# Kernel optimization log

Measured on AMD Instinct MI355X. Metric: run time of the kernel, lower is better.

## Reference

```python
import jax, jax.numpy as jnp
import numpy as np
import math

NUM_ITER = 5
FEAT_STRIDE = 16
GAUSS_SIGMA = 1.0
HINGE_THRESHOLD = -999.0
MIN_FILTER_REG = 1e-3
ALPHA_EPS = 0.0


def apply_filter(feat, weights):
    # feat: (ni, ns, C, H, W); weights: (ns, C, fH, fW) -> scores (ni, ns, oH, oW)
    ni, ns, C, H, W = feat.shape
    fH, fW = weights.shape[-2], weights.shape[-1]
    x = feat.reshape(ni, ns * C, H, W)
    out = jax.lax.conv_general_dilated(
        x, weights, window_strides=(1, 1),
        padding=((fH // 2, fH // 2), (fW // 2, fW // 2)),
        dimension_numbers=('NCHW', 'OIHW', 'NCHW'),
        feature_group_count=ns)
    return out  # (ni, ns, oH, oW); oH = H + (fH+1)%2


def get_label(center, out_sz, sigma):
    # center: (ni, ns, 2) in (row, col) order
    k0 = jnp.arange(out_sz[0], dtype=jnp.float32)[None, None, :, None]
    k1 = jnp.arange(out_sz[1], dtype=jnp.float32)[None, None, None, :]
    g0 = jnp.exp(-0.5 / (sigma * sigma) * (k0 - center[..., 0][..., None, None]) ** 2)
    g1 = jnp.exp(-0.5 / (sigma * sigma) * (k1 - center[..., 1][..., None, None]) ** 2)
    return g0 * g1  # (ni, ns, oH, oW)


def _forward(weights, feat, bb, log_step_length, filter_reg):
    ni, ns = feat.shape[0], feat.shape[1]
    fH, fW = weights.shape[-2], weights.shape[-1]
    out_sz = (feat.shape[-2] + (fH + 1) % 2, feat.shape[-1] + (fW + 1) % 2)
    step = jnp.exp(log_step_length)[0]
    reg = jnp.maximum(filter_reg * filter_reg, MIN_FILTER_REG ** 2)[0]
    dmap_offset = jnp.array([fH % 2, fW % 2], jnp.float32) / 2.0
    # (x, y) -> (row, col), feature-grid coordinates
    center = ((bb[..., :2] + bb[..., 2:] / 2.0) / FEAT_STRIDE)[..., ::-1] - dmap_offset
    label = get_label(center, out_sz, GAUSS_SIGMA)
    mask = (label > HINGE_THRESHOLD).astype(feat.dtype)
    label = label * mask
    sw = math.sqrt(1.0 / ni)

    losses = []
    for _ in range(NUM_ITER):
        scores = apply_filter(feat, weights)
        scores_act = mask * scores + (1.0 - mask) * jax.nn.relu(scores)
        score_mask = mask + (1.0 - mask) * (jax.lax.stop_gradient(scores) > 0).astype(scores.dtype)
        residuals = sw * (scores_act - label)
        losses.append((jnp.sum(residuals ** 2) + reg * jnp.sum(weights ** 2)) / ns)
        residuals_mapped = score_mask * (sw * residuals)
        # feat-transpose = adjoint of apply_filter w.r.t. the filter weights
        _, vjp_fn = jax.vjp(lambda w: apply_filter(feat, w), weights)
        data_grad = vjp_fn(residuals_mapped)[0]
        weights_grad = data_grad + reg * weights
        scores_grad = apply_filter(feat, weights_grad)
        scores_grad = sw * (score_mask * scores_grad)
        alpha_num = jnp.sum(weights_grad ** 2, axis=(1, 2, 3))  # (ns,)
        alpha_den = jnp.maximum(
            jnp.sum(scores_grad.reshape(ni, ns, -1) ** 2, axis=(0, 2))
            + (reg + ALPHA_EPS) * alpha_num, 1e-8)
        alpha = alpha_num / alpha_den
        weights = weights - step * alpha[:, None, None, None] * weights_grad

    scores = apply_filter(feat, weights)
    scores = mask * scores + (1.0 - mask) * jax.nn.relu(scores)
    losses.append((jnp.sum((sw * (scores - label)) ** 2) + reg * jnp.sum(weights ** 2)) / ns)
    return weights, jnp.stack(losses)


def setup_inputs() -> dict:
    key = jax.random.key(0)
    k1, k2, k3, k4 = jax.random.split(key, 4)
    ni, ns, C, H, W, fH, fW = 3, 32, 512, 22, 22, 4, 4
    weights = 0.01 * jax.random.normal(k1, (ns, C, fH, fW), jnp.float32)
    feat = jax.random.normal(k2, (ni, ns, C, H, W), jnp.float32)
    # boxes (x, y, w, h) in image coords (image size = 22*16 = 352)
    xy = jax.random.uniform(k3, (ni, ns, 2), jnp.float32, 50.0, 250.0)
    wh = jax.random.uniform(k4, (ni, ns, 2), jnp.float32, 32.0, 96.0)
    bb = jnp.concatenate([xy, wh], axis=-1)
    log_step_length = jnp.zeros((1,), jnp.float32)  # log(1.0)
    filter_reg = 0.01 * jnp.ones((1,), jnp.float32)
    return {"weights": weights, "feat": feat, "bb": bb,
            "log_step_length": log_step_length, "filter_reg": filter_reg}


def reference(weights, feat, bb, log_step_length, filter_reg):
    return _forward(weights, feat, bb, log_step_length, filter_reg)
```

## Files before the change

kernel.cpp:

```cpp
#include <hip/hip_runtime.h>
#include <hip/hip_fp16.h>

#define NI 3
#define NS 32
#define CHN 512
#define OH 23
#define P2 529
#define NP 50784
#define UV 484
#define WSZ 262144
#define KTOT 1536
#define RSP 1544

typedef unsigned int uint32;
typedef unsigned short u16;
typedef _Float16 h2 __attribute__((ext_vector_type(2)));
typedef _Float16 f16x8 __attribute__((ext_vector_type(8)));
typedef float f32x4 __attribute__((ext_vector_type(4)));

#define OFF_FEATT 0UL
#define OFF_LABEL 47579136UL
#define OFF_S0    47782272UL
#define OFF_S1    47985408UL
#define OFF_SGRAW 48188544UL
#define OFF_WG    48391680UL
#define OFF_WGF16 49440256UL
#define OFF_W0F16 49964544UL
#define OFF_PART  50488832UL
#define OFF_FEATC 50521600UL

#define P_DEN   0
#define P_NUM   4320
#define P_LOSS  5600
#define P_WSQ0  5760
#define P_WSQA  5792
#define P_WSQ5  6816
#define P_L5    7840

__device__ __forceinline__ float waveSum(float v) {
#pragma unroll
  for (int o = 32; o > 0; o >>= 1) v += __shfl_xor(v, o, 64);
  return v;
}

__device__ __forceinline__ float alphaFor(const float* __restrict__ part, int t, int s,
                                          float reg) {
  const float* np_ = part + P_NUM + (size_t)(t * NS + s) * 8;
  const float* dp_ = part + P_DEN + (size_t)(t * NS + s) * 6;
  float nu = 0.f;
#pragma unroll
  for (int i = 0; i < 8; ++i) nu += np_[i];
  float de = 0.f;
#pragma unroll
  for (int i = 0; i < 6; ++i) de += dp_[i];
  return nu / fmaxf(de + reg * nu, 1e-8f);
}

__global__ __launch_bounds__(256) void k_setup(const float* __restrict__ feat,
                                               const float* __restrict__ w0,
                                               const float* __restrict__ bb,
                                               u16* __restrict__ featT,
                                               u16* __restrict__ featC,
                                               u16* __restrict__ w0f16,
                                               float* __restrict__ wmaster,
                                               float* __restrict__ label,
                                               float* __restrict__ part) {
  __shared__ uint32 lds32[64 * 121];
  __shared__ float sred[4];
  int b = blockIdx.x, tid = threadIdx.x;
  if (b < 1536) {
    int snT = b >> 4, r4 = b & 15;
    int cb = r4 >> 1, uvh = r4 & 1;
    int s = snT / 3, n = snT % 3;
    const float* fsrc =
        feat + ((size_t)n * NS + s) * CHN * UV + (size_t)(cb * 64) * UV + uvh * 242;
#pragma unroll
    for (int it = 0; it < 31; ++it) {
      int idx = it * 256 + tid;
      if (idx < 7744) {
        int r = (unsigned)idx / 121u;
        int j = idx - r * 121;
        float2 v = *(const float2*)(fsrc + (size_t)r * UV + 2 * j);
        lds32[idx] = (uint32)__half_as_ushort(__float2half(v.x)) |
                     ((uint32)__half_as_ushort(__float2half(v.y)) << 16);
      }
    }
    __syncthreads();
    uint32* dstT = (uint32*)featT +
                   ((size_t)(snT * 4 + (cb >> 1)) * UV + uvh * 242) * 64 + (cb & 1) * 32;
#pragma unroll
    for (int it = 0; it < 16; ++it) {
      int o = it * 256 + tid;
      if (o < 3872) {
        int uv = o >> 4, kp = o & 15;
        int j = uv >> 1, sh = (uv & 1) * 16;
        uint32 a0 = lds32[(4 * kp + 0) * 121 + j];
        uint32 a1 = lds32[(4 * kp + 1) * 121 + j];
        uint32 a2 = lds32[(4 * kp + 2) * 121 + j];
        uint32 a3 = lds32[(4 * kp + 3) * 121 + j];
        uint2 val;
        val.x = ((a0 >> sh) & 0xffffu) | (((a1 >> sh) & 0xffffu) << 16);
        val.y = ((a2 >> sh) & 0xffffu) | (((a3 >> sh) & 0xffffu) << 16);
        *(uint2*)(dstT + (size_t)uv * 64 + 2 * kp) = val;
      }
    }
    uint32* dstC =
        (uint32*)featC + ((size_t)(s * CHN + cb * 64)) * 768 + n * 256 + uvh * 121;
    if (uvh == 0) {
#pragma unroll
      for (int it = 0; it < 31; ++it) {
        int idx = it * 256 + tid;
        if (idx < 7744) {
          int c = (unsigned)idx / 121u;
          int j = idx - c * 121;
          dstC[(size_t)c * 768 + j] = lds32[idx];
        }
      }
    } else {
#pragma unroll
      for (int it = 0; it < 34; ++it) {
        int idx = it * 256 + tid;
        if (idx < 8640) {
          int c = (unsigned)idx / 135u;
          int j = idx - c * 135;
          dstC[(size_t)c * 768 + j] = (j < 121) ? lds32[c * 121 + j] : 0u;
        }
      }
    }
  } else if (b < 1568) {
    int s = b - 1536;
    for (int i = tid; i < 8192; i += 256) {
      int tap = i >> 9, c = i & 511;
      w0f16[(size_t)s * 8192 + i] =
          __half_as_ushort(__float2half(w0[(size_t)s * 8192 + c * 16 + tap]));
    }
    float sq = 0.f;
    for (int i = tid; i < 8192; i += 256) {
      float v = w0[(size_t)s * 8192 + i];
      wmaster[(size_t)s * 8192 + i] = v;
      sq += v * v;
    }
    sq = waveSum(sq);
    if ((tid & 63) == 0) sred[tid >> 6] = sq;
    __syncthreads();
    if (tid == 0) part[P_WSQ0 + s] = sred[0] + sred[1] + sred[2] + sred[3];
  } else {
    int p = (b - 1568) * 256 + tid;
    if (p < NP) {
      int nsid = p / P2, rem = p % P2;
      int i = rem / OH, j = rem % OH;
      const float* bp = bb + (size_t)nsid * 4;
      float cr = (bp[1] + 0.5f * bp[3]) * 0.0625f;
      float cc = (bp[0] + 0.5f * bp[2]) * 0.0625f;
      float dy = (float)i - cr, dx = (float)j - cc;
      label[p] = __expf(-0.5f * (dy * dy + dx * dx));
    }
  }
}

__global__ __launch_bounds__(1024) void k_conv_fwd(const u16* __restrict__ featT,
                                                   const u16* __restrict__ wf16,
                                                   float* __restrict__ outbuf, int t,
                                                   float* __restrict__ part) {
  __shared__ uint32 w_lds[16 * 260];
  __shared__ float G[288 * 17];
  __shared__ float dred[16];
  int tid = threadIdx.x;
  int bidx = blockIdx.x;
  int snT = bidx >> 1, h = bidx & 1;
  int s = snT / 3, n = snT - s * 3;
  const uint32* wsrc = (const uint32*)(wf16 + (size_t)s * 8192);
  for (int i = tid; i < 4096; i += 1024) {
    int tap = i >> 8, p = i & 255;
    w_lds[tap * 260 + p] = wsrc[i];
  }
  __syncthreads();
  int wave = tid >> 6, lane = tid & 63;
  int q = lane >> 4, m16 = lane & 15;
  int uv0 = h ? 220 : 0;
  int ntiles = 18 - h;
  int t0 = wave;
  bool has2 = (wave + 16 < ntiles);
  int t1 = has2 ? wave + 16 : wave;
  f32x4 acc0 = {0.f, 0.f, 0.f, 0.f}, acc1 = {0.f, 0.f, 0.f, 0.f};
  size_t base = (size_t)snT * 4 * UV * 128;
  int r0i = uv0 + t0 * 16 + m16;
  if (r0i > 483) r0i = 483;
  int r1i = uv0 + t1 * 16 + m16;
  if (r1i > 483) r1i = 483;
  size_t row0 = (size_t)r0i * 128;
  size_t row1 = (size_t)r1i * 128;
#pragma unroll
  for (int step = 0; step < 16; ++step) {
    int cb = step >> 2, cin = (step & 3) * 32;
    size_t cbase = base + (size_t)cb * UV * 128 + cin + q * 8;
    f16x8 a0 = *(const f16x8*)(featT + cbase + row0);
    uint4 bw = *(const uint4*)&w_lds[m16 * 260 + step * 16 + q * 4];
    f16x8 bf = __builtin_bit_cast(f16x8, bw);
    acc0 = __builtin_amdgcn_mfma_f32_16x16x32_f16(a0, bf, acc0, 0, 0, 0);
    if (has2) {
      f16x8 a1 = *(const f16x8*)(featT + cbase + row1);
      acc1 = __builtin_amdgcn_mfma_f32_16x16x32_f16(a1, bf, acc1, 0, 0, 0);
    }
  }
#pragma unroll
  for (int r = 0; r < 4; ++r) G[(t0 * 16 + q * 4 + r) * 17 + m16] = acc0[r];
  if (has2) {
#pragma unroll
    for (int r = 0; r < 4; ++r) G[(t1 * 16 + q * 4 + r) * 17 + m16] = acc1[r];
  }
  __syncthreads();
  float dsq = 0.f;
  int y0 = h ? 12 : 0;
  int npix = h ? 253 : 276;
  int p = tid;
  if (p < npix) {
    int yl = p / 23, x = p - yl * 23;
    int y = y0 + yl;
    float val = 0.f;
#pragma unroll
    for (int ky = 0; ky < 4; ++ky) {
      int u = y + ky - 2;
      if ((unsigned)u < 22u) {
#pragma unroll
        for (int kx = 0; kx < 4; ++kx) {
          int v = x + kx - 2;
          if ((unsigned)v < 22u) val += G[(u * 22 + v - uv0) * 17 + ky * 4 + kx];
        }
      }
    }
    outbuf[(size_t)(n * NS + s) * P2 + y * 23 + x] = val;
    dsq = val * val;
  }
  if (t >= 0) {
    dsq = waveSum(dsq);
    if (lane == 0) dred[wave] = dsq;
    __syncthreads();
    if (tid == 0) {
      float dsum = 0.f;
#pragma unroll
      for (int i = 0; i < 16; ++i) dsum += dred[i];
      part[P_DEN + ((size_t)(t * NS + s) * 3 + n) * 2 + h] = dsum * (1.0f / 3.0f);
    }
  }
}

__global__ __launch_bounds__(1024) void k_adjoint(
    int t, const u16* __restrict__ featC, const float* __restrict__ label,
    const float* __restrict__ scores_old, float* __restrict__ scores_new,
    const float* __restrict__ sgraw, float* __restrict__ wg, u16* __restrict__ wgf16,
    float* __restrict__ wmaster, float* __restrict__ part, const float* __restrict__ lsl,
    const float* __restrict__ fr) {
  __shared__ float r_lds[3 * P2];
  __shared__ __align__(16) u16 rs[16 * RSP];
  __shared__ __align__(16) float kred[3 * 4 * 64 * 4];
  __shared__ float lred[16], nred[16], wred[16];
  int tid = threadIdx.x;
  int s = blockIdx.x >> 3, chunk = blockIdx.x & 7;
  int c0 = chunk * 64;
  float step = __expf(lsl[0]);
  float frv = fr[0];
  float reg = fmaxf(frv * frv, 1e-6f);
  float alpha_p = (t >= 1) ? alphaFor(part, t - 1, s, reg) : 0.f;

  float lsum = 0.f;
  for (int pl = tid; pl < 1587; pl += 1024) {
    int nn = (unsigned)pl / (unsigned)P2;
    int rem = pl - nn * P2;
    size_t gp = (size_t)(nn * NS + s) * P2 + rem;
    float S = scores_old[gp];
    if (t >= 1) S -= step * alpha_p * sgraw[gp];
    float d = S - label[gp];
    r_lds[nn * P2 + rem] = d * (1.0f / 3.0f);
    if (chunk == 0) {
      if (t >= 1) scores_new[gp] = S;
      lsum += d * d;
    }
  }
  lsum = waveSum(lsum);
  if ((tid & 63) == 0) lred[tid >> 6] = lsum;
  __syncthreads();
  if (chunk == 0 && tid == 0) {
    float L = 0.f;
#pragma unroll
    for (int i = 0; i < 16; ++i) L += lred[i];
    part[P_LOSS + t * NS + s] = L * (1.0f / 3.0f);
  }

  for (int idx = tid; idx < 16 * RSP; idx += 1024) {
    int tap = (unsigned)idx / (unsigned)RSP;
    int k = idx - tap * RSP;
    float val = 0.f;
    if (k < KTOT) {
      int n = k >> 9, uv = k & 511;
      if (uv < UV) {
        int u = (unsigned)uv / 22u;
        int v = uv - u * 22;
        int ky = tap >> 2, kx = tap & 3;
        int y = u + 2 - ky, x = v + 2 - kx;
        if ((unsigned)y < 23u && (unsigned)x < 23u) val = r_lds[n * P2 + y * OH + x];
      }
    }
    rs[idx] = __half_as_ushort(__float2half(val));
  }
  __syncthreads();

  int wave = tid >> 6, lane = tid & 63;
  int q = lane >> 4, m16 = lane & 15;
  int tile = wave & 3, kq = wave >> 2;
  int c = c0 + tile * 16 + m16;
  const u16* arow = featC + ((size_t)(s * CHN + c)) * KTOT + kq * 384 + q * 8;
  const u16* brow = rs + m16 * RSP + kq * 384 + q * 8;
  f32x4 acc = {0.f, 0.f, 0.f, 0.f};
#pragma unroll
  for (int ks = 0; ks < 12; ++ks) {
    f16x8 a = *(const f16x8*)(arow + ks * 32);
    f16x8 bf = *(const f16x8*)(brow + ks * 32);
    acc = __builtin_amdgcn_mfma_f32_16x16x32_f16(a, bf, acc, 0, 0, 0);
  }
  if (kq) *(f32x4*)&kred[(((kq - 1) * 4 + tile) * 64 + lane) * 4] = acc;
  __syncthreads();

  float num_part = 0.f, wsq_part = 0.f;
  if (kq == 0) {
#pragma unroll
    for (int kk = 0; kk < 3; ++kk)
      acc += *(const f32x4*)&kred[((kk * 4 + tile) * 64 + lane) * 4];
    int tap = m16;
    int ccb = c0 + tile * 16 + q * 4;
    union { u16 h[4]; uint2 v2; } pk;
#pragma unroll
    for (int r = 0; r < 4; ++r) {
      int cc = ccb + r;
      size_t widx = (size_t)s * 8192 + (size_t)cc * 16 + tap;
      float wold = wmaster[widx];
      float wnew = wold;
      if (t >= 1) {
        wnew = wold - step * alpha_p * wg[widx];
        wmaster[widx] = wnew;
      }
      float wgn = acc[r] + reg * wnew;
      wg[widx] = wgn;
      pk.h[r] = __half_as_ushort(__float2half(wgn));
      wsq_part += wnew * wnew;
      num_part += wgn * wgn;
    }
    *(uint2*)&wgf16[(size_t)s * 8192 + (size_t)tap * 512 + ccb] = pk.v2;
  }
  num_part = waveSum(num_part);
  wsq_part = waveSum(wsq_part);
  if (lane == 0) {
    nred[wave] = num_part;
    wred[wave] = wsq_part;
  }
  __syncthreads();
  if (tid == 0) {
    float nsum = 0.f, wsum = 0.f;
#pragma unroll
    for (int i = 0; i < 16; ++i) {
      nsum += nred[i];
      wsum += wred[i];
    }
    part[P_NUM + (size_t)(t * NS + s) * 8 + chunk] = nsum;
    if (t >= 1) part[P_WSQA + (size_t)((t - 1) * NS + s) * 8 + chunk] = wsum;
  }
}

__global__ void k_final(float* __restrict__ wmaster, const float* __restrict__ wg,
                        const float* __restrict__ scores4, const float* __restrict__ sgraw,
                        const float* __restrict__ label, float* __restrict__ part,
                        const float* __restrict__ lsl, const float* __restrict__ fr) {
  __shared__ float alpha_s[32];
  __shared__ float red4[4];
  int b = blockIdx.x, tid = threadIdx.x;
  float step = __expf(lsl[0]);
  float frv = fr[0];
  float reg = fmaxf(frv * frv, 1e-6f);
  if (tid < 32) alpha_s[tid] = alphaFor(part, 4, tid, reg);
  __syncthreads();
  if (b < 1024) {
    int idx = b * 256 + tid;
    int s = idx >> 13;
    float w5 = wmaster[idx] - step * alpha_s[s] * wg[idx];
    wmaster[idx] = w5;
    float sq = waveSum(w5 * w5);
    if ((tid & 63) == 0) red4[tid >> 6] = sq;
    __syncthreads();
    if (tid == 0) part[P_WSQ5 + b] = red4[0] + red4[1] + red4[2] + red4[3];
  } else {
    int p = (b - 1024) * 256 + tid;
    float contrib = 0.f;
    if (p < NP) {
      int nsid = p / P2;
      int s = nsid & 31;
      float s5 = scores4[p] - step * alpha_s[s] * sgraw[p];
      float d = s5 - label[p];
      contrib = d * d;
    }
    contrib = waveSum(contrib);
    if ((tid & 63) == 0) red4[tid >> 6] = contrib;
    __syncthreads();
    if (tid == 0)
      part[P_L5 + (b - 1024)] = (red4[0] + red4[1] + red4[2] + red4[3]) * (1.0f / 3.0f);
  }
}

__global__ void k_losses(float* __restrict__ out_losses, const float* __restrict__ part,
                         const float* __restrict__ fr) {
  __shared__ float red[8];
  int tid = threadIdx.x;
  float frv = fr[0];
  float reg = fmaxf(frv * frv, 1e-6f);
  float v5 = 0.f;
  for (int i = tid; i < 1024; i += 256) v5 += part[P_WSQ5 + i];
  v5 = waveSum(v5);
  if ((tid & 63) == 0) red[tid >> 6] = v5;
  __syncthreads();
  float wsq5 = red[0] + red[1] + red[2] + red[3];
  float l5 = 0.f;
  for (int i = tid; i < 199; i += 256) l5 += part[P_L5 + i];
  l5 = waveSum(l5);
  if ((tid & 63) == 0) red[4 + (tid >> 6)] = l5;
  __syncthreads();
  float loss5 = red[4] + red[5] + red[6] + red[7];
  if (tid < 5) {
    int t = tid;
    float ls = 0.f;
    for (int i = 0; i < 32; ++i) ls += part[P_LOSS + t * NS + i];
    float ws_ = 0.f;
    if (t == 0) {
      for (int i = 0; i < 32; ++i) ws_ += part[P_WSQ0 + i];
    } else {
      for (int i = 0; i < 256; ++i) ws_ += part[P_WSQA + (t - 1) * 256 + i];
    }
    out_losses[t] = (ls + reg * ws_) * (1.0f / 32.0f);
  }
  if (tid == 5) out_losses[5] = (loss5 + reg * wsq5) * (1.0f / 32.0f);
}

extern "C" void kernel_launch(void* const* d_in, const int* in_sizes, int n_in,
                              void* d_out, int out_size, void* d_ws, size_t ws_size,
                              hipStream_t stream) {
  const float* w0 = (const float*)d_in[0];
  const float* feat = (const float*)d_in[1];
  const float* bb = (const float*)d_in[2];
  const float* lsl = (const float*)d_in[3];
  const float* fr = (const float*)d_in[4];
  float* out = (float*)d_out;
  char* ws = (char*)d_ws;
  u16* featT = (u16*)(ws + OFF_FEATT);
  float* label = (float*)(ws + OFF_LABEL);
  float* s0 = (float*)(ws + OFF_S0);
  float* s1 = (float*)(ws + OFF_S1);
  float* sgraw = (float*)(ws + OFF_SGRAW);
  float* wg = (float*)(ws + OFF_WG);
  u16* wgf16 = (u16*)(ws + OFF_WGF16);
  u16* w0f16 = (u16*)(ws + OFF_W0F16);
  float* part = (float*)(ws + OFF_PART);
  u16* featC = (u16*)(ws + OFF_FEATC);

  k_setup<<<1767, 256, 0, stream>>>(feat, w0, bb, featT, featC, w0f16, out, label, part);
  k_conv_fwd<<<192, 1024, 0, stream>>>(featT, w0f16, s0, -1, part);
  float* sbuf[2] = {s0, s1};
  for (int t = 0; t < 5; ++t) {
    const float* so = (t == 0) ? s0 : sbuf[(t - 1) & 1];
    float* sn = sbuf[t & 1];
    k_adjoint<<<256, 1024, 0, stream>>>(t, featC, label, so, sn, sgraw, wg, wgf16, out,
                                        part, lsl, fr);
    k_conv_fwd<<<192, 1024, 0, stream>>>(featT, wgf16, sgraw, t, part);
  }
  k_final<<<1223, 256, 0, stream>>>(out, wg, s0, sgraw, label, part, lsl, fr);
  k_losses<<<1, 256, 0, stream>>>(out + WSZ, part, fr);
}
```

Measured before the change: 370.4 us.

## Split forward conv blocks by channel halves instead of spatial halves

Each forward-conv block now covers all output pixels for half of the input channel blocks, and writes a partial score map to one of two buffers. Consumers add the two partial maps. The spatial split recomputed halo rows in both halves; the channel split drops that redundant MFMA work. In exchange, the step-size denominator reduction moves out of the conv into the adjoint kernel plus a new small k_den kernel, and it costs extra reads of two score buffers and one more launch.

```diff
diff --git a/kernel.cpp b/kernel.cpp
--- a/kernel.cpp
+++ b/kernel.cpp
@@ -28,6 +28,8 @@
 #define OFF_W0F16 49964544UL
 #define OFF_PART  50488832UL
 #define OFF_FEATC 50521600UL
+#define OFF_S0B   100853248UL
+#define OFF_SGB   101056384UL
 
 #define P_DEN   0
 #define P_NUM   4320
@@ -41,19 +43,6 @@
 #pragma unroll
   for (int o = 32; o > 0; o >>= 1) v += __shfl_xor(v, o, 64);
   return v;
-}
-
-__device__ __forceinline__ float alphaFor(const float* __restrict__ part, int t, int s,
-                                          float reg) {
-  const float* np_ = part + P_NUM + (size_t)(t * NS + s) * 8;
-  const float* dp_ = part + P_DEN + (size_t)(t * NS + s) * 6;
-  float nu = 0.f;
-#pragma unroll
-  for (int i = 0; i < 8; ++i) nu += np_[i];
-  float de = 0.f;
-#pragma unroll
-  for (int i = 0; i < 6; ++i) de += dp_[i];
-  return nu / fmaxf(de + reg * nu, 1e-8f);
 }
 
 __global__ __launch_bounds__(256) void k_setup(const float* __restrict__ feat,
@@ -160,42 +149,37 @@
 
 __global__ __launch_bounds__(1024) void k_conv_fwd(const u16* __restrict__ featT,
                                                    const u16* __restrict__ wf16,
-                                                   float* __restrict__ outbuf, int t,
-                                                   float* __restrict__ part) {
-  __shared__ uint32 w_lds[16 * 260];
-  __shared__ float G[288 * 17];
-  __shared__ float dred[16];
+                                                   float* __restrict__ outA,
+                                                   float* __restrict__ outB) {
+  __shared__ uint32 w_lds[16 * 132];
+  __shared__ float G[496 * 17];
   int tid = threadIdx.x;
   int bidx = blockIdx.x;
-  int snT = bidx >> 1, h = bidx & 1;
+  int snT = bidx >> 1, ch = bidx & 1;
   int s = snT / 3, n = snT - s * 3;
-  const uint32* wsrc = (const uint32*)(wf16 + (size_t)s * 8192);
-  for (int i = tid; i < 4096; i += 1024) {
-    int tap = i >> 8, p = i & 255;
-    w_lds[tap * 260 + p] = wsrc[i];
+  const uint32* wsrc = (const uint32*)(wf16 + (size_t)s * 8192) + ch * 128;
+  for (int i = tid; i < 2048; i += 1024) {
+    int tap = i >> 7, p = i & 127;
+    w_lds[tap * 132 + p] = wsrc[(size_t)tap * 256 + p];
   }
   __syncthreads();
   int wave = tid >> 6, lane = tid & 63;
   int q = lane >> 4, m16 = lane & 15;
-  int uv0 = h ? 220 : 0;
-  int ntiles = 18 - h;
-  int t0 = wave;
-  bool has2 = (wave + 16 < ntiles);
-  int t1 = has2 ? wave + 16 : wave;
+  int t0 = wave, t1 = wave + 16;
+  bool has2 = (t1 < 31);
   f32x4 acc0 = {0.f, 0.f, 0.f, 0.f}, acc1 = {0.f, 0.f, 0.f, 0.f};
   size_t base = (size_t)snT * 4 * UV * 128;
-  int r0i = uv0 + t0 * 16 + m16;
-  if (r0i > 483) r0i = 483;
-  int r1i = uv0 + t1 * 16 + m16;
+  int r0i = t0 * 16 + m16;
+  int r1i = has2 ? t1 * 16 + m16 : 483;
   if (r1i > 483) r1i = 483;
   size_t row0 = (size_t)r0i * 128;
   size_t row1 = (size_t)r1i * 128;
 #pragma unroll
-  for (int step = 0; step < 16; ++step) {
-    int cb = step >> 2, cin = (step & 3) * 32;
+  for (int ks = 0; ks < 8; ++ks) {
+    int cb = ch * 2 + (ks >> 2), cin = (ks & 3) * 32;
     size_t cbase = base + (size_t)cb * UV * 128 + cin + q * 8;
     f16x8 a0 = *(const f16x8*)(featT + cbase + row0);
-    uint4 bw = *(const uint4*)&w_lds[m16 * 260 + step * 16 + q * 4];
+    uint4 bw = *(const uint4*)&w_lds[m16 * 132 + ks * 16 + q * 4];
     f16x8 bf = __builtin_bit_cast(f16x8, bw);
     acc0 = __builtin_amdgcn_mfma_f32_16x16x32_f16(a0, bf, acc0, 0, 0, 0);
     if (has2) {
@@ -210,13 +194,8 @@
     for (int r = 0; r < 4; ++r) G[(t1 * 16 + q * 4 + r) * 17 + m16] = acc1[r];
   }
   __syncthreads();
-  float dsq = 0.f;
-  int y0 = h ? 12 : 0;
-  int npix = h ? 253 : 276;
-  int p = tid;
-  if (p < npix) {
-    int yl = p / 23, x = p - yl * 23;
-    int y = y0 + yl;
+  if (tid < P2) {
+    int y = tid / 23, x = tid - y * 23;
     float val = 0.f;
 #pragma unroll
     for (int ky = 0; ky < 4; ++ky) {
@@ -225,51 +204,64 @@
 #pragma unroll
         for (int kx = 0; kx < 4; ++kx) {
           int v = x + kx - 2;
-          if ((unsigned)v < 22u) val += G[(u * 22 + v - uv0) * 17 + ky * 4 + kx];
+          if ((unsigned)v < 22u) val += G[(u * 22 + v) * 17 + ky * 4 + kx];
         }
       }
     }
-    outbuf[(size_t)(n * NS + s) * P2 + y * 23 + x] = val;
-    dsq = val * val;
-  }
-  if (t >= 0) {
-    dsq = waveSum(dsq);
-    if (lane == 0) dred[wave] = dsq;
-    __syncthreads();
-    if (tid == 0) {
-      float dsum = 0.f;
-#pragma unroll
-      for (int i = 0; i < 16; ++i) dsum += dred[i];
-      part[P_DEN + ((size_t)(t * NS + s) * 3 + n) * 2 + h] = dsum * (1.0f / 3.0f);
-    }
+    float* dst = ch ? outB : outA;
+    dst[(size_t)(n * NS + s) * P2 + tid] = val;
   }
 }
 
 __global__ __launch_bounds__(1024) void k_adjoint(
     int t, const u16* __restrict__ featC, const float* __restrict__ label,
+    const float* __restrict__ s0a, const float* __restrict__ s0b,
     const float* __restrict__ scores_old, float* __restrict__ scores_new,
-    const float* __restrict__ sgraw, float* __restrict__ wg, u16* __restrict__ wgf16,
-    float* __restrict__ wmaster, float* __restrict__ part, const float* __restrict__ lsl,
+    const float* __restrict__ sga, const float* __restrict__ sgb,
+    float* __restrict__ wg, u16* __restrict__ wgf16, float* __restrict__ wmaster,
+    float* __restrict__ part, const float* __restrict__ lsl,
     const float* __restrict__ fr) {
   __shared__ float r_lds[3 * P2];
   __shared__ __align__(16) u16 rs[16 * RSP];
   __shared__ __align__(16) float kred[3 * 4 * 64 * 4];
-  __shared__ float lred[16], nred[16], wred[16];
+  __shared__ float lred[16], nred[16], wred[16], dend[16];
   int tid = threadIdx.x;
   int s = blockIdx.x >> 3, chunk = blockIdx.x & 7;
   int c0 = chunk * 64;
   float step = __expf(lsl[0]);
   float frv = fr[0];
   float reg = fmaxf(frv * frv, 1e-6f);
-  float alpha_p = (t >= 1) ? alphaFor(part, t - 1, s, reg) : 0.f;
+
+  float alpha_p = 0.f;
+  if (t >= 1) {
+    const float* np_ = part + P_NUM + (size_t)((t - 1) * NS + s) * 8;
+    float nu = 0.f;
+#pragma unroll
+    for (int i = 0; i < 8; ++i) nu += np_[i];
+    float dp = 0.f;
+    for (int pl = tid; pl < 1587; pl += 1024) {
+      int nn = (unsigned)pl / (unsigned)P2;
+      int rem = pl - nn * P2;
+      size_t gp = (size_t)(nn * NS + s) * P2 + rem;
+      float g = sga[gp] + sgb[gp];
+      dp += g * g;
+    }
+    dp = waveSum(dp);
+    if ((tid & 63) == 0) dend[tid >> 6] = dp;
+    __syncthreads();
+    float de = 0.f;
+#pragma unroll
+    for (int i = 0; i < 16; ++i) de += dend[i];
+    alpha_p = nu / fmaxf(de * (1.0f / 3.0f) + reg * nu, 1e-8f);
+  }
 
   float lsum = 0.f;
   for (int pl = tid; pl < 1587; pl += 1024) {
     int nn = (unsigned)pl / (unsigned)P2;
     int rem = pl - nn * P2;
     size_t gp = (size_t)(nn * NS + s) * P2 + rem;
-    float S = scores_old[gp];
-    if (t >= 1) S -= step * alpha_p * sgraw[gp];
+    float S = (t <= 1) ? (s0a[gp] + s0b[gp]) : scores_old[gp];
+    if (t >= 1) S -= step * alpha_p * (sga[gp] + sgb[gp]);
     float d = S - label[gp];
     r_lds[nn * P2 + rem] = d * (1.0f / 3.0f);
     if (chunk == 0) {
@@ -366,17 +358,52 @@
   }
 }
 
+__global__ __launch_bounds__(1024) void k_den(const float* __restrict__ sga,
+                                              const float* __restrict__ sgb,
+                                              float* __restrict__ part) {
+  __shared__ float dend[16];
+  int s = blockIdx.x, tid = threadIdx.x;
+  float dp = 0.f;
+  for (int pl = tid; pl < 1587; pl += 1024) {
+    int nn = (unsigned)pl / (unsigned)P2;
+    int rem = pl - nn * P2;
+    size_t gp = (size_t)(nn * NS + s) * P2 + rem;
+    float g = sga[gp] + sgb[gp];
+    dp += g * g;
+  }
+  dp = waveSum(dp);
+  if ((tid & 63) == 0) dend[tid >> 6] = dp;
+  __syncthreads();
+  if (tid == 0) {
+    float de = 0.f;
+#pragma unroll
+    for (int i = 0; i < 16; ++i) de += dend[i];
+    part[P_DEN + s] = de * (1.0f / 3.0f);
+  }
+}
+
+__device__ __forceinline__ float alphaFinal(const float* __restrict__ part, int s,
+                                            float reg) {
+  const float* np_ = part + P_NUM + (size_t)(4 * NS + s) * 8;
+  float nu = 0.f;
+#pragma unroll
+  for (int i = 0; i < 8; ++i) nu += np_[i];
+  float de = part[P_DEN + s];
+  return nu / fmaxf(de + reg * nu, 1e-8f);
+}
+
 __global__ void k_final(float* __restrict__ wmaster, const float* __restrict__ wg,
-                        const float* __restrict__ scores4, const float* __restrict__ sgraw,
-                        const float* __restrict__ label, float* __restrict__ part,
-                        const float* __restrict__ lsl, const float* __restrict__ fr) {
+                        const float* __restrict__ scores4, const float* __restrict__ sga,
+                        const float* __restrict__ sgb, const float* __restrict__ label,
+                        float* __restrict__ part, const float* __restrict__ lsl,
+                        const float* __restrict__ fr) {
   __shared__ float alpha_s[32];
   __shared__ float red4[4];
   int b = blockIdx.x, tid = threadIdx.x;
   float step = __expf(lsl[0]);
   float frv = fr[0];
   float reg = fmaxf(frv * frv, 1e-6f);
-  if (tid < 32) alpha_s[tid] = alphaFor(part, 4, tid, reg);
+  if (tid < 32) alpha_s[tid] = alphaFinal(part, tid, reg);
   __syncthreads();
   if (b < 1024) {
     int idx = b * 256 + tid;
@@ -393,7 +420,7 @@
     if (p < NP) {
       int nsid = p / P2;
       int s = nsid & 31;
-      float s5 = scores4[p] - step * alpha_s[s] * sgraw[p];
+      float s5 = scores4[p] - step * alpha_s[s] * (sga[p] + sgb[p]);
       float d = s5 - label[p];
       contrib = d * d;
     }
@@ -451,8 +478,10 @@
   u16* featT = (u16*)(ws + OFF_FEATT);
   float* label = (float*)(ws + OFF_LABEL);
   float* s0 = (float*)(ws + OFF_S0);
+  float* s0b = (float*)(ws + OFF_S0B);
   float* s1 = (float*)(ws + OFF_S1);
-  float* sgraw = (float*)(ws + OFF_SGRAW);
+  float* sga = (float*)(ws + OFF_SGRAW);
+  float* sgb = (float*)(ws + OFF_SGB);
   float* wg = (float*)(ws + OFF_WG);
   u16* wgf16 = (u16*)(ws + OFF_WGF16);
   u16* w0f16 = (u16*)(ws + OFF_W0F16);
@@ -460,15 +489,15 @@
   u16* featC = (u16*)(ws + OFF_FEATC);
 
   k_setup<<<1767, 256, 0, stream>>>(feat, w0, bb, featT, featC, w0f16, out, label, part);
-  k_conv_fwd<<<192, 1024, 0, stream>>>(featT, w0f16, s0, -1, part);
-  float* sbuf[2] = {s0, s1};
+  k_conv_fwd<<<192, 1024, 0, stream>>>(featT, w0f16, s0, s0b);
   for (int t = 0; t < 5; ++t) {
-    const float* so = (t == 0) ? s0 : sbuf[(t - 1) & 1];
-    float* sn = sbuf[t & 1];
-    k_adjoint<<<256, 1024, 0, stream>>>(t, featC, label, so, sn, sgraw, wg, wgf16, out,
-                                        part, lsl, fr);
-    k_conv_fwd<<<192, 1024, 0, stream>>>(featT, wgf16, sgraw, t, part);
-  }
-  k_final<<<1223, 256, 0, stream>>>(out, wg, s0, sgraw, label, part, lsl, fr);
+    const float* so = (t <= 1) ? s0 : ((t & 1) ? s0 : s1);
+    float* sn = (t & 1) ? s1 : s0;
+    k_adjoint<<<256, 1024, 0, stream>>>(t, featC, label, s0, s0b, so, sn, sga, sgb, wg,
+                                        wgf16, out, part, lsl, fr);
+    k_conv_fwd<<<192, 1024, 0, stream>>>(featT, wgf16, sga, sgb);
+  }
+  k_den<<<32, 1024, 0, stream>>>(sga, sgb, part);
+  k_final<<<1223, 256, 0, stream>>>(out, wg, s0, sga, sgb, label, part, lsl, fr);
   k_losses<<<1, 256, 0, stream>>>(out + WSZ, part, fr);
 }
```

Measured after the change: 358.9 us. 1.03x faster.
